# Kernel tuning notes

Hardware: AMD Instinct MI355X
Metric: run time of the kernel (lower is better)

## Reference

```python
import jax, jax.numpy as jnp
import numpy as np
import math

D_MODEL = 768
NHEAD = 12
NUM_LAYERS = 6
INPUT_DIM = 768
HEAD_DIM = D_MODEL // NHEAD
D_FF = 4 * D_MODEL
TOTAL_HEADS = NUM_LAYERS * NHEAD
B, N = 4, 512


def _ln(x, g, b, eps=1e-5):
    mu = jnp.mean(x, axis=-1, keepdims=True)
    var = jnp.mean((x - mu) ** 2, axis=-1, keepdims=True)
    return (x - mu) * jax.lax.rsqrt(var + eps) * g + b


def setup_inputs() -> dict:
    key = jax.random.key(0)
    ks = iter(jax.random.split(key, 32))
    s = 0.02  # init scale keeps sigmoid scores away from saturation
    d = {
        "sentence_embeddings": jax.random.normal(next(ks), (B, N, INPUT_DIM), jnp.float32),
        "Win": jax.random.normal(next(ks), (D_MODEL, INPUT_DIM), jnp.float32) * s,
        "b_in": jnp.zeros((D_MODEL,), jnp.float32),
        "Wq": jax.random.normal(next(ks), (NUM_LAYERS, D_MODEL, D_MODEL), jnp.float32) * s,
        "bq": jnp.zeros((NUM_LAYERS, D_MODEL), jnp.float32),
        "Wk": jax.random.normal(next(ks), (NUM_LAYERS, D_MODEL, D_MODEL), jnp.float32) * s,
        "bk": jnp.zeros((NUM_LAYERS, D_MODEL), jnp.float32),
        "Wv": jax.random.normal(next(ks), (NUM_LAYERS, D_MODEL, D_MODEL), jnp.float32) * s,
        "bv": jnp.zeros((NUM_LAYERS, D_MODEL), jnp.float32),
        "Wo": jax.random.normal(next(ks), (NUM_LAYERS, D_MODEL, D_MODEL), jnp.float32) * s,
        "bo": jnp.zeros((NUM_LAYERS, D_MODEL), jnp.float32),
        "g1": jnp.ones((NUM_LAYERS, D_MODEL), jnp.float32),
        "be1": jnp.zeros((NUM_LAYERS, D_MODEL), jnp.float32),
        "g2": jnp.ones((NUM_LAYERS, D_MODEL), jnp.float32),
        "be2": jnp.zeros((NUM_LAYERS, D_MODEL), jnp.float32),
        "W1": jax.random.normal(next(ks), (NUM_LAYERS, D_FF, D_MODEL), jnp.float32) * s,
        "bf1": jnp.zeros((NUM_LAYERS, D_FF), jnp.float32),
        "W2": jax.random.normal(next(ks), (NUM_LAYERS, D_MODEL, D_FF), jnp.float32) * s,
        "bf2": jnp.zeros((NUM_LAYERS, D_MODEL), jnp.float32),
        "Wr1": jax.random.normal(next(ks), (D_MODEL // 2, D_MODEL), jnp.float32) * s,
        "br1": jnp.zeros((D_MODEL // 2,), jnp.float32),
        "Wr2": jax.random.normal(next(ks), (TOTAL_HEADS, D_MODEL // 2), jnp.float32) * s,
        "br2": jnp.zeros((TOTAL_HEADS,), jnp.float32),
        "agg_bias": jnp.zeros((1,), jnp.float32),
    }
    return d


def _forward(sentence_embeddings, Win, b_in, Wq, bq, Wk, bk, Wv, bv, Wo, bo,
             g1, be1, g2, be2, W1, bf1, W2, bf2, Wr1, br1, Wr2, br2, agg_bias):
    b, n, _ = sentence_embeddings.shape
    x = sentence_embeddings @ Win.T + b_in  # [B,N,D]
    off_diag = (1.0 - jnp.eye(n, dtype=x.dtype))[None, None]  # [1,1,N,N]
    scale = 1.0 / math.sqrt(HEAD_DIM)
    all_scores = []
    for i in range(NUM_LAYERS):
        n1 = _ln(x, g1[i], be1[i])
        q = (n1 @ Wq[i].T + bq[i]).reshape(b, n, NHEAD, HEAD_DIM).transpose(0, 2, 1, 3)
        k = (n1 @ Wk[i].T + bk[i]).reshape(b, n, NHEAD, HEAD_DIM).transpose(0, 2, 1, 3)
        v = (n1 @ Wv[i].T + bv[i]).reshape(b, n, NHEAD, HEAD_DIM).transpose(0, 2, 1, 3)
        scores = jnp.einsum('bhnd,bhmd->bhnm', q, k) * scale
        probs = jax.nn.sigmoid(scores)  # [B,H,N,N]
        row_sums = probs.sum(axis=-1, keepdims=True) + 1e-6
        attn = jnp.einsum('bhnm,bhmd->bhnd', probs, v) / row_sums
        attn = attn.transpose(0, 2, 1, 3).reshape(b, n, D_MODEL)
        x = x + attn @ Wo[i].T + bo[i]
        n2 = _ln(x, g2[i], be2[i])
        ff = jax.nn.gelu(n2 @ W1[i].T + bf1[i], approximate=False) @ W2[i].T + bf2[i]
        x = x + ff
        all_scores.append(probs * off_diag)  # zero the diagonal
    raw_w = jax.nn.gelu(x @ Wr1.T + br1, approximate=False) @ Wr2.T + br2  # [B,N,LH]
    stacked = jnp.concatenate(all_scores, axis=1)  # [B, L*H, N, N]
    final = jnp.einsum('bnh,bhnm->bnm', raw_w, stacked)
    return final + agg_bias[0]


def reference(sentence_embeddings, Win, b_in, Wq, bq, Wk, bk, Wv, bv, Wo, bo,
              g1, be1, g2, be2, W1, bf1, W2, bf2, Wr1, br1, Wr2, br2, agg_bias):
    return _forward(sentence_embeddings, Win, b_in, Wq, bq, Wk, bk, Wv, bv, Wo, bo,
                    g1, be1, g2, be2, W1, bf1, W2, bf2, Wr1, br1, Wr2, br2, agg_bias)
```

## Files before the change

### kernel.cpp

```cpp
#include <hip/hip_runtime.h>
#include <stdint.h>

#define LAYERS 6
#define BB 4
#define NSEQ 512
#define DM 768
#define NH 12
#define HD 64
#define DFF 3072
#define MTOK 2048
#define QKVN 2304
#define DR1 384
#define TH 72

typedef __attribute__((ext_vector_type(8))) short bf16x8;
typedef __attribute__((ext_vector_type(4))) float f32x4;

__device__ __forceinline__ unsigned short f2bf(float f) {
  union { float f; uint32_t u; } v; v.f = f;
  return (unsigned short)((v.u + 0x7fffu + ((v.u >> 16) & 1u)) >> 16);
}
__device__ __forceinline__ float bf2f(unsigned short h) {
  union { uint32_t u; float f; } v; v.u = ((uint32_t)h) << 16;
  return v.f;
}
__device__ __forceinline__ void gload16(const void* g, void* l) {
  __builtin_amdgcn_global_load_lds((const __attribute__((address_space(1))) void*)g,
                                   (__attribute__((address_space(3))) void*)l, 16, 0, 0);
}
#define MFMA(a, b, c) __builtin_amdgcn_mfma_f32_16x16x32_bf16(a, b, c, 0, 0, 0)

__device__ __forceinline__ float sigmoid8(float s) {
  float e, r;
  float t = s * -0.18033688011112443f;
  asm("v_exp_f32 %0, %1" : "=v"(e) : "v"(t));
  float d = 1.0f + e;
  asm("v_rcp_f32 %0, %1" : "=v"(r) : "v"(d));
  return r;
}

__device__ __forceinline__ float gelu_f(float x) {
  float t = 0.7978845608028654f * x * (1.0f + 0.044715f * x * x);
  float u = fminf(t * 2.8853900817779268f, 126.0f);
  float e, r;
  asm("v_exp_f32 %0, %1" : "=v"(e) : "v"(u));
  float d = e + 1.0f;
  asm("v_rcp_f32 %0, %1" : "=v"(r) : "v"(d));
  return x * e * r;
}

__global__ void cvt_f32_bf16(const float* __restrict__ s, unsigned short* __restrict__ d, int n4) {
  int i = blockIdx.x * blockDim.x + threadIdx.x;
  if (i >= n4) return;
  float4 v = reinterpret_cast<const float4*>(s)[i];
  ushort4 o;
  o.x = f2bf(v.x); o.y = f2bf(v.y); o.z = f2bf(v.z); o.w = f2bf(v.w);
  reinterpret_cast<ushort4*>(d)[i] = o;
}

__global__ void convert_all(const float* __restrict__ Wq, const float* __restrict__ Wk,
                            const float* __restrict__ Wv, const float* __restrict__ Wo,
                            const float* __restrict__ W1, const float* __restrict__ W2,
                            const float* __restrict__ bqA, const float* __restrict__ bkA,
                            const float* __restrict__ bvA,
                            unsigned short* __restrict__ qkvw6, float* __restrict__ qkvb6,
                            unsigned short* __restrict__ wow6, unsigned short* __restrict__ w1w6,
                            unsigned short* __restrict__ w2w6) {
  const int A4 = (QKVN * DM) / 4;
  const int B4 = (DM * DM) / 4;
  const int C4 = (DFF * DM) / 4;
  const int l = blockIdx.y;
  const float* wq = Wq + (size_t)l * DM * DM;
  const float* wk = Wk + (size_t)l * DM * DM;
  const float* wv = Wv + (size_t)l * DM * DM;
  const float* wo = Wo + (size_t)l * DM * DM;
  const float* w1 = W1 + (size_t)l * DFF * DM;
  const float* w2 = W2 + (size_t)l * DM * DFF;
  unsigned short* qkvw = qkvw6 + (size_t)l * QKVN * DM;
  unsigned short* wow  = wow6  + (size_t)l * DM * DM;
  unsigned short* w1w  = w1w6  + (size_t)l * DFF * DM;
  unsigned short* w2w  = w2w6  + (size_t)l * DM * DFF;
  float* qkvb = qkvb6 + (size_t)l * QKVN;
  int i = blockIdx.x * blockDim.x + threadIdx.x;
  if (i < QKVN / 4) {
    int j = i * 4;
    #pragma unroll
    for (int t = 0; t < 4; ++t) {
      int jj = j + t;
      int seg = jj / DM, c = jj % DM;
      const float* src = (seg == 0) ? (bqA + l * DM) : ((seg == 1) ? (bkA + l * DM) : (bvA + l * DM));
      qkvb[jj] = src[c];
    }
  }
  const float* s4; unsigned short* dst;
  if (i < A4) {
    int j = i * 4; int row = j / DM; int c = j % DM;
    const float* w = (row < DM) ? wq : ((row < 2 * DM) ? wk : wv);
    s4 = w + (size_t)(row % DM) * DM + c; dst = qkvw + j;
  } else if (i < A4 + B4) {
    int j = (i - A4) * 4; s4 = wo + j; dst = wow + j;
  } else if (i < A4 + B4 + C4) {
    int j = (i - A4 - B4) * 4; s4 = w1 + j; dst = w1w + j;
  } else if (i < A4 + B4 + 2 * C4) {
    int j = (i - A4 - B4 - C4) * 4; s4 = w2 + j; dst = w2w + j;
  } else return;
  float4 v = *reinterpret_cast<const float4*>(s4);
  ushort4 o;
  o.x = f2bf(v.x); o.y = f2bf(v.y); o.z = f2bf(v.z); o.w = f2bf(v.w);
  *reinterpret_cast<ushort4*>(dst) = o;
}

__global__ __launch_bounds__(256) void ln_kernel(const float* __restrict__ x,
                                                 const float* __restrict__ g,
                                                 const float* __restrict__ b,
                                                 unsigned short* __restrict__ out) {
  int wave = threadIdx.x >> 6;
  int lane = threadIdx.x & 63;
  int row = blockIdx.x * 4 + wave;
  const float* xr = x + (size_t)row * DM;
  float v[12];
  #pragma unroll
  for (int c = 0; c < 3; ++c) {
    float4 t = *reinterpret_cast<const float4*>(xr + lane * 12 + c * 4);
    v[c * 4 + 0] = t.x; v[c * 4 + 1] = t.y; v[c * 4 + 2] = t.z; v[c * 4 + 3] = t.w;
  }
  float s = 0.f, s2 = 0.f;
  #pragma unroll
  for (int c = 0; c < 12; ++c) { s += v[c]; s2 += v[c] * v[c]; }
  #pragma unroll
  for (int m = 1; m < 64; m <<= 1) { s += __shfl_xor(s, m); s2 += __shfl_xor(s2, m); }
  float mu = s * (1.f / 768.f);
  float var = s2 * (1.f / 768.f) - mu * mu;
  float rstd = rsqrtf(var + 1e-5f);
  unsigned short o[12];
  #pragma unroll
  for (int c = 0; c < 12; ++c) {
    int col = lane * 12 + c;
    o[c] = f2bf((v[c] - mu) * rstd * g[col] + b[col]);
  }
  unsigned short* orow = out + (size_t)row * DM + lane * 12;
  #pragma unroll
  for (int c = 0; c < 3; ++c)
    reinterpret_cast<ushort4*>(orow)[c] = make_ushort4(o[c * 4], o[c * 4 + 1], o[c * 4 + 2], o[c * 4 + 3]);
}

__global__ __launch_bounds__(256) void ff2_ln(const float* __restrict__ pk,
                                              const float* __restrict__ bias,
                                              float* __restrict__ x,
                                              const float* __restrict__ g,
                                              const float* __restrict__ b,
                                              unsigned short* __restrict__ out,
                                              int last) {
  int wave = threadIdx.x >> 6;
  int lane = threadIdx.x & 63;
  int row = blockIdx.x * 4 + wave;
  size_t base = (size_t)row * DM;
  float v[12];
  #pragma unroll
  for (int c = 0; c < 3; ++c) {
    int col = lane * 12 + c * 4;
    float4 xv = *reinterpret_cast<const float4*>(x + base + col);
    float4 p0 = *reinterpret_cast<const float4*>(pk + base + col);
    float4 p1 = *reinterpret_cast<const float4*>(pk + (size_t)MTOK * DM + base + col);
    float4 bb = *reinterpret_cast<const float4*>(bias + col);
    v[c * 4 + 0] = xv.x + p0.x + p1.x + bb.x;
    v[c * 4 + 1] = xv.y + p0.y + p1.y + bb.y;
    v[c * 4 + 2] = xv.z + p0.z + p1.z + bb.z;
    v[c * 4 + 3] = xv.w + p0.w + p1.w + bb.w;
  }
  #pragma unroll
  for (int c = 0; c < 3; ++c) {
    float4 o = {v[c * 4], v[c * 4 + 1], v[c * 4 + 2], v[c * 4 + 3]};
    *reinterpret_cast<float4*>(x + base + lane * 12 + c * 4) = o;
  }
  unsigned short o[12];
  if (last) {
    #pragma unroll
    for (int c = 0; c < 12; ++c) o[c] = f2bf(v[c]);
  } else {
    float s = 0.f, s2 = 0.f;
    #pragma unroll
    for (int c = 0; c < 12; ++c) { s += v[c]; s2 += v[c] * v[c]; }
    #pragma unroll
    for (int m = 1; m < 64; m <<= 1) { s += __shfl_xor(s, m); s2 += __shfl_xor(s2, m); }
    float mu = s * (1.f / 768.f);
    float var = s2 * (1.f / 768.f) - mu * mu;
    float rstd = rsqrtf(var + 1e-5f);
    #pragma unroll
    for (int c = 0; c < 12; ++c) {
      int col = lane * 12 + c;
      o[c] = f2bf((v[c] - mu) * rstd * g[col] + b[col]);
    }
  }
  unsigned short* orow = out + base + lane * 12;
  #pragma unroll
  for (int c = 0; c < 3; ++c)
    reinterpret_cast<ushort4*>(orow)[c] = make_ushort4(o[c * 4], o[c * 4 + 1], o[c * 4 + 2], o[c * 4 + 3]);
}

template<int BM, int BN, int EPI>
__global__ __launch_bounds__(256) void gemm_bt(const unsigned short* __restrict__ A,
                                               const unsigned short* __restrict__ B,
                                               const float* __restrict__ bias,
                                               const float* __restrict__ resid,
                                               float* __restrict__ outf,
                                               unsigned short* __restrict__ outb,
                                               int M, int N, int K) {
  constexpr int MI = BM / 32;
  constexpr int NI = BN / 32;
  constexpr int ACH = BM / 32;
  constexpr int BCH = BN / 32;
  __shared__ unsigned short As[2][BM * 64];
  __shared__ unsigned short Bs[2][BN * 64];
  const int tid = threadIdx.x;
  const int w = tid >> 6, lane = tid & 63;
  const int wr = w >> 1, wc = w & 1;
  const int l15 = lane & 15, rq = lane >> 4;
  const int bM = blockIdx.y * BM, bN = blockIdx.x * BN;
  const f32x4 zero4 = {0.f, 0.f, 0.f, 0.f};
  f32x4 acc[MI][NI];
  #pragma unroll
  for (int mi = 0; mi < MI; ++mi)
    #pragma unroll
    for (int ni = 0; ni < NI; ++ni) acc[mi][ni] = zero4;
  const int srow = lane >> 3;
  const int scol = ((lane & 7) ^ (lane >> 3)) * 8;
  auto stage = [&](int bf, int k0) {
    #pragma unroll
    for (int cc = 0; cc < ACH; ++cc) {
      int c = w * ACH + cc;
      gload16(A + (size_t)(bM + 8 * c + srow) * K + k0 + scol, (void*)(&As[bf][c * 512]));
    }
    #pragma unroll
    for (int cc = 0; cc < BCH; ++cc) {
      int c = w * BCH + cc;
      gload16(B + (size_t)(bN + 8 * c + srow) * K + k0 + scol, (void*)(&Bs[bf][c * 512]));
    }
  };
  const int kper = K / gridDim.z;
  const int kbase = blockIdx.z * kper;
  const int nt = kper / 64;
  stage(0, kbase);
  __syncthreads();
  int buf = 0;
  for (int t = 0; t < nt; ++t) {
    if (t + 1 < nt) stage(buf ^ 1, kbase + (t + 1) * 64);
    #pragma unroll
    for (int kk = 0; kk < 2; ++kk) {
      bf16x8 af[MI], bfr[NI];
      #pragma unroll
      for (int mi = 0; mi < MI; ++mi) {
        int row = wr * (BM / 2) + mi * 16 + l15;
        af[mi] = *(const bf16x8*)(&As[buf][row * 64 + (((kk * 4 + rq) ^ (row & 7)) * 8)]);
      }
      #pragma unroll
      for (int ni = 0; ni < NI; ++ni) {
        int row = wc * (BN / 2) + ni * 16 + l15;
        bfr[ni] = *(const bf16x8*)(&Bs[buf][row * 64 + (((kk * 4 + rq) ^ (row & 7)) * 8)]);
      }
      #pragma unroll
      for (int mi = 0; mi < MI; ++mi)
        #pragma unroll
        for (int ni = 0; ni < NI; ++ni)
          acc[mi][ni] = MFMA(af[mi], bfr[ni], acc[mi][ni]);
    }
    __syncthreads();
    buf ^= 1;
  }
  #pragma unroll
  for (int mi = 0; mi < MI; ++mi)
    #pragma unroll
    for (int ni = 0; ni < NI; ++ni)
      #pragma unroll
      for (int r = 0; r < 4; ++r) {
        int row = bM + wr * (BM / 2) + mi * 16 + 4 * rq + r;
        int col = bN + wc * (BN / 2) + ni * 16 + l15;
        if constexpr (EPI == 4) {
          outf[(size_t)blockIdx.z * M * N + (size_t)row * N + col] = acc[mi][ni][r];
        } else {
          float val = acc[mi][ni][r] + bias[col];
          if constexpr (EPI == 0) {
            outb[(size_t)row * N + col] = f2bf(val);
          } else if constexpr (EPI == 1) {
            outb[(size_t)row * N + col] = f2bf(gelu_f(val));
          } else if constexpr (EPI == 2) {
            outf[(size_t)row * N + col] = resid[(size_t)row * N + col] + val;
          } else {
            outf[(size_t)row * N + col] = val;
          }
        }
      }
}

__global__ __launch_bounds__(256) void attn_kernel(const unsigned short* __restrict__ qkv,
                                                   float* __restrict__ po,
                                                   float* __restrict__ prs) {
  __shared__ unsigned short Ks[64 * 64];
  __shared__ unsigned short vt[64 * 72];
  __shared__ unsigned short pl[4][16 * 72];
  const int tid = threadIdx.x;
  const int w = tid >> 6, lane = tid & 63;
  const int l15 = lane & 15, rq = lane >> 4;
  const int b = blockIdx.y / NH, h = blockIdx.y % NH;
  const int n0 = blockIdx.x * 64;
  const int part = blockIdx.z;
  const unsigned short* base = qkv + (size_t)(b * NSEQ) * QKVN + h * HD;
  bf16x8 aq0, aq1;
  {
    const unsigned short* qp = base + (size_t)(n0 + w * 16 + l15) * QKVN + rq * 8;
    aq0 = *(const bf16x8*)qp;
    aq1 = *(const bf16x8*)(qp + 32);
  }
  float rs[4] = {0.f, 0.f, 0.f, 0.f};
  const f32x4 zero4 = {0.f, 0.f, 0.f, 0.f};
  f32x4 acco[4];
  #pragma unroll
  for (int j = 0; j < 4; ++j) acco[j] = zero4;
  unsigned short* plw = &pl[w][0];

  for (int mt = 0; mt < 4; ++mt) {
    const int m0 = part * 256 + mt * 64;
    __syncthreads();
    #pragma unroll
    for (int it = 0; it < 2; ++it) {
      int idx = tid + it * 256;
      int r = idx >> 3, c = idx & 7;
      bf16x8 kv = *(const bf16x8*)(base + 768 + (size_t)(m0 + r) * QKVN + c * 8);
      *(bf16x8*)(Ks + r * 64 + (c ^ (r & 7)) * 8) = kv;
      int cd = idx & 63, g = (idx >> 6) & 7;
      const unsigned short* vp = base + 1536 + (size_t)(m0 + g * 8) * QKVN + cd;
      bf16x8 vv;
      #pragma unroll
      for (int j = 0; j < 8; ++j) vv[j] = (short)vp[(size_t)j * QKVN];
      *(bf16x8*)(vt + cd * 72 + g * 8) = vv;
    }
    __syncthreads();
    #pragma unroll
    for (int ni = 0; ni < 4; ++ni) {
      int kr = ni * 16 + l15;
      bf16x8 bk0 = *(const bf16x8*)(Ks + kr * 64 + ((rq) ^ (kr & 7)) * 8);
      bf16x8 bk1 = *(const bf16x8*)(Ks + kr * 64 + ((rq + 4) ^ (kr & 7)) * 8);
      f32x4 z = zero4;
      z = MFMA(aq0, bk0, z);
      z = MFMA(aq1, bk1, z);
      #pragma unroll
      for (int r = 0; r < 4; ++r) {
        float p = sigmoid8(z[r]);
        rs[r] += p;
        plw[(4 * rq + r) * 72 + ni * 16 + l15] = f2bf(p);
      }
    }
    #pragma unroll
    for (int kk = 0; kk < 2; ++kk) {
      bf16x8 ap = *(const bf16x8*)(plw + l15 * 72 + kk * 32 + rq * 8);
      #pragma unroll
      for (int j2 = 0; j2 < 4; ++j2) {
        bf16x8 bvv = *(const bf16x8*)(vt + (j2 * 16 + l15) * 72 + kk * 32 + rq * 8);
        acco[j2] = MFMA(ap, bvv, acco[j2]);
      }
    }
  }
  #pragma unroll
  for (int m = 1; m < 16; m <<= 1)
    #pragma unroll
    for (int r = 0; r < 4; ++r) rs[r] += __shfl_xor(rs[r], m);
  float* pop = po + (size_t)part * MTOK * DM;
  #pragma unroll
  for (int j2 = 0; j2 < 4; ++j2)
    #pragma unroll
    for (int r = 0; r < 4; ++r) {
      int row = b * NSEQ + n0 + w * 16 + 4 * rq + r;
      int col = h * HD + j2 * 16 + l15;
      pop[(size_t)row * DM + col] = acco[j2][r];
    }
  if (l15 == 0) {
    #pragma unroll
    for (int r = 0; r < 4; ++r)
      prs[((size_t)part * (BB * NH) + blockIdx.y) * NSEQ + n0 + w * 16 + 4 * rq + r] = rs[r];
  }
}

__global__ __launch_bounds__(256) void attn_combine(const float* __restrict__ po,
                                                    const float* __restrict__ prs,
                                                    unsigned short* __restrict__ attnbf) {
  int i = blockIdx.x * 256 + threadIdx.x;
  int e = i * 4;
  int row = e / DM, col = e % DM;
  int b = row >> 9, n = row & 511, h = col >> 6;
  float r0 = prs[((size_t)(b * NH + h)) * NSEQ + n];
  float r1 = prs[(size_t)(BB * NH) * NSEQ + ((size_t)(b * NH + h)) * NSEQ + n];
  float inv = 1.f / (r0 + r1 + 1e-6f);
  float4 p0 = *reinterpret_cast<const float4*>(po + e);
  float4 p1 = *reinterpret_cast<const float4*>(po + (size_t)MTOK * DM + e);
  ushort4 o;
  o.x = f2bf((p0.x + p1.x) * inv);
  o.y = f2bf((p0.y + p1.y) * inv);
  o.z = f2bf((p0.z + p1.z) * inv);
  o.w = f2bf((p0.w + p1.w) * inv);
  *reinterpret_cast<ushort4*>(attnbf + e) = o;
}

__global__ __launch_bounds__(128) void wr2_kernel(const unsigned short* __restrict__ h1,
                                                  const float* __restrict__ wr2,
                                                  const float* __restrict__ br2,
                                                  float* __restrict__ raww) {
  __shared__ float hrow[DR1];
  int row = blockIdx.x;
  const unsigned short* hp = h1 + (size_t)row * DR1;
  for (int c = threadIdx.x; c < DR1; c += 128) hrow[c] = bf2f(hp[c]);
  __syncthreads();
  int j = threadIdx.x;
  if (j < TH) {
    const float* wrow = wr2 + (size_t)j * DR1;
    float acc = 0.f;
    for (int c4 = 0; c4 < DR1 / 4; ++c4) {
      float4 hv = *reinterpret_cast<const float4*>(hrow + c4 * 4);
      float4 wv = *reinterpret_cast<const float4*>(wrow + c4 * 4);
      acc += hv.x * wv.x + hv.y * wv.y + hv.z * wv.z + hv.w * wv.w;
    }
    raww[(size_t)row * TH + j] = acc + br2[j];
  }
}

__global__ __launch_bounds__(256) void agg_kernel(const unsigned short* __restrict__ qkv_all,
                                                  const float* __restrict__ raww,
                                                  float* __restrict__ part) {
  __shared__ unsigned short Ks[64 * 64];
  __shared__ unsigned short Qs[64 * 64];
  const int tid = threadIdx.x;
  const int w = tid >> 6, lane = tid & 63;
  const int l15 = lane & 15, rq = lane >> 4;
  const int z = blockIdx.z;
  const int l = z >> 2, b = z & 3;
  const int m0 = blockIdx.x * 64, nb = blockIdx.y * 64;
  const unsigned short* base = qkv_all + (size_t)l * MTOK * QKVN + (size_t)(b * NSEQ) * QKVN;
  const f32x4 zero4 = {0.f, 0.f, 0.f, 0.f};
  float acc[4][4];
  #pragma unroll
  for (int ni = 0; ni < 4; ++ni)
    #pragma unroll
    for (int r = 0; r < 4; ++r) acc[ni][r] = 0.f;
  for (int h = 0; h < NH; ++h) {
    __syncthreads();
    #pragma unroll
    for (int it = 0; it < 2; ++it) {
      int idx = tid + it * 256;
      int r = idx >> 3, c = idx & 7;
      bf16x8 kv = *(const bf16x8*)(base + (size_t)(m0 + r) * QKVN + 768 + h * HD + c * 8);
      *(bf16x8*)(Ks + r * 64 + (c ^ (r & 7)) * 8) = kv;
      bf16x8 qv = *(const bf16x8*)(base + (size_t)(nb + r) * QKVN + h * HD + c * 8);
      *(bf16x8*)(Qs + r * 64 + (c ^ (r & 7)) * 8) = qv;
    }
    __syncthreads();
    const int qr = w * 16 + l15;
    bf16x8 aq0 = *(const bf16x8*)(Qs + qr * 64 + ((rq) ^ (qr & 7)) * 8);
    bf16x8 aq1 = *(const bf16x8*)(Qs + qr * 64 + ((rq + 4) ^ (qr & 7)) * 8);
    float wl[4];
    #pragma unroll
    for (int r = 0; r < 4; ++r)
      wl[r] = raww[(size_t)(b * NSEQ + nb + w * 16 + 4 * rq + r) * TH + l * NH + h];
    #pragma unroll
    for (int ni = 0; ni < 4; ++ni) {
      int kr = ni * 16 + l15;
      bf16x8 bk0 = *(const bf16x8*)(Ks + kr * 64 + ((rq) ^ (kr & 7)) * 8);
      bf16x8 bk1 = *(const bf16x8*)(Ks + kr * 64 + ((rq + 4) ^ (kr & 7)) * 8);
      f32x4 zz = zero4;
      zz = MFMA(aq0, bk0, zz);
      zz = MFMA(aq1, bk1, zz);
      #pragma unroll
      for (int r = 0; r < 4; ++r) {
        acc[ni][r] += wl[r] * sigmoid8(zz[r]);
      }
    }
  }
  #pragma unroll
  for (int ni = 0; ni < 4; ++ni)
    #pragma unroll
    for (int r = 0; r < 4; ++r) {
      int n = nb + w * 16 + 4 * rq + r;
      part[((size_t)z * NSEQ + n) * NSEQ + m0 + ni * 16 + l15] = acc[ni][r];
    }
}

__global__ __launch_bounds__(256) void agg_reduce(const float* __restrict__ part,
                                                  const float* __restrict__ agg_bias,
                                                  float* __restrict__ out) {
  int i = blockIdx.x * 256 + threadIdx.x;
  int e = i * 4;
  float4 s = {0.f, 0.f, 0.f, 0.f};
  #pragma unroll
  for (int l = 0; l < LAYERS; ++l) {
    float4 p = *reinterpret_cast<const float4*>(part + (size_t)l * BB * NSEQ * NSEQ + e);
    s.x += p.x; s.y += p.y; s.z += p.z; s.w += p.w;
  }
  int n = (e >> 9) & 511, m = e & 511;
  float ab = agg_bias[0];
  float4 o;
  o.x = (n == m)     ? ab : s.x + ab;
  o.y = (n == m + 1) ? ab : s.y + ab;
  o.z = (n == m + 2) ? ab : s.z + ab;
  o.w = (n == m + 3) ? ab : s.w + ab;
  *reinterpret_cast<float4*>(out + e) = o;
}

extern "C" void kernel_launch(void* const* d_in, const int* in_sizes, int n_in,
                              void* d_out, int out_size, void* d_ws, size_t ws_size,
                              hipStream_t stream) {
  const float* emb  = (const float*)d_in[0];
  const float* Win  = (const float*)d_in[1];
  const float* b_in = (const float*)d_in[2];
  const float* Wq   = (const float*)d_in[3];
  const float* bq   = (const float*)d_in[4];
  const float* Wk   = (const float*)d_in[5];
  const float* bk   = (const float*)d_in[6];
  const float* Wv   = (const float*)d_in[7];
  const float* bv   = (const float*)d_in[8];
  const float* Wo   = (const float*)d_in[9];
  const float* bo   = (const float*)d_in[10];
  const float* g1   = (const float*)d_in[11];
  const float* be1  = (const float*)d_in[12];
  const float* g2   = (const float*)d_in[13];
  const float* be2  = (const float*)d_in[14];
  const float* W1   = (const float*)d_in[15];
  const float* bf1  = (const float*)d_in[16];
  const float* W2   = (const float*)d_in[17];
  const float* bf2  = (const float*)d_in[18];
  const float* Wr1  = (const float*)d_in[19];
  const float* br1  = (const float*)d_in[20];
  const float* Wr2  = (const float*)d_in[21];
  const float* br2  = (const float*)d_in[22];
  const float* aggb = (const float*)d_in[23];
  float* out = (float*)d_out;
  (void)in_sizes; (void)n_in; (void)out_size; (void)ws_size;

  char* ws = (char*)d_ws;
  size_t off = 0;
  auto alloc = [&](size_t bytes) -> char* {
    char* p = ws + off;
    off += (bytes + 255) & ~(size_t)255;
    return p;
  };
  unsigned short* qkvw6  = (unsigned short*)alloc((size_t)LAYERS * QKVN * DM * 2);
  float*          qkvb6  = (float*)alloc((size_t)LAYERS * QKVN * 4);
  unsigned short* wow6   = (unsigned short*)alloc((size_t)LAYERS * DM * DM * 2);
  unsigned short* w1w6   = (unsigned short*)alloc((size_t)LAYERS * DFF * DM * 2);
  unsigned short* w2w6   = (unsigned short*)alloc((size_t)LAYERS * DM * DFF * 2);
  unsigned short* winw   = (unsigned short*)alloc((size_t)DM * DM * 2);
  unsigned short* wr1w   = (unsigned short*)alloc((size_t)DR1 * DM * 2);
  unsigned short* h1bf   = (unsigned short*)alloc((size_t)MTOK * DR1 * 2);
  float*          raww   = (float*)alloc((size_t)MTOK * TH * 4);
  float*          prs    = (float*)alloc((size_t)2 * BB * NH * NSEQ * 4);
  float*          skbuf  = (float*)alloc((size_t)2 * MTOK * DM * 4);
  unsigned short* qkvall = (unsigned short*)alloc((size_t)LAYERS * MTOK * QKVN * 2);
  char* scratch = alloc(0);
  unsigned short* embbf  = (unsigned short*)(scratch);
  float*          x      = (float*)(scratch + 3145728);
  unsigned short* nbf    = (unsigned short*)(scratch + 3145728 + 6291456);
  unsigned short* attnbf = (unsigned short*)(scratch + 3145728 + 6291456 + 3145728);
  char*           S      = scratch + 3145728 + 6291456 + 3145728 + 3145728;
  unsigned short* xbf    = (unsigned short*)(S + 12582912);
  float*          po     = (float*)S;
  unsigned short* ff1bf  = (unsigned short*)S;
  float*          part   = (float*)scratch;

  cvt_f32_bf16<<<1536, 256, 0, stream>>>(emb, embbf, (MTOK * DM) / 4);
  cvt_f32_bf16<<<576, 256, 0, stream>>>(Win, winw, (DM * DM) / 4);
  cvt_f32_bf16<<<288, 256, 0, stream>>>(Wr1, wr1w, (DR1 * DM) / 4);

  const int CL_GRID = ((QKVN * DM + DM * DM + 2 * DFF * DM) / 4 + 255) / 256;
  convert_all<<<dim3(CL_GRID, LAYERS), 256, 0, stream>>>(Wq, Wk, Wv, Wo, W1, W2, bq, bk, bv,
                                                         qkvw6, qkvb6, wow6, w1w6, w2w6);

  dim3 g768(DM / 64, MTOK / 64);
  gemm_bt<64, 64, 3><<<g768, 256, 0, stream>>>(embbf, winw, b_in, nullptr, x, nullptr, MTOK, DM, DM);
  ln_kernel<<<512, 256, 0, stream>>>(x, g1, be1, nbf);

  for (int l = 0; l < LAYERS; ++l) {
    unsigned short* qkvl = qkvall + (size_t)l * MTOK * QKVN;
    dim3 gqkv(QKVN / 128, MTOK / 64);
    gemm_bt<64, 128, 0><<<gqkv, 256, 0, stream>>>(nbf, qkvw6 + (size_t)l * QKVN * DM,
                                                  qkvb6 + (size_t)l * QKVN, nullptr, nullptr,
                                                  qkvl, MTOK, QKVN, DM);
    attn_kernel<<<dim3(8, BB * NH, 2), 256, 0, stream>>>(qkvl, po, prs);
    attn_combine<<<(MTOK * DM / 4) / 256, 256, 0, stream>>>(po, prs, attnbf);
    gemm_bt<64, 64, 2><<<g768, 256, 0, stream>>>(attnbf, wow6 + (size_t)l * DM * DM,
                                                 bo + l * DM, x, x, nullptr, MTOK, DM, DM);
    ln_kernel<<<512, 256, 0, stream>>>(x, g2 + l * DM, be2 + l * DM, nbf);
    dim3 gff1(DFF / 128, MTOK / 64);
    gemm_bt<64, 128, 1><<<gff1, 256, 0, stream>>>(nbf, w1w6 + (size_t)l * DFF * DM,
                                                  bf1 + l * DFF, nullptr, nullptr, ff1bf,
                                                  MTOK, DFF, DM);
    dim3 gff2(DM / 64, MTOK / 64, 2);
    gemm_bt<64, 64, 4><<<gff2, 256, 0, stream>>>(ff1bf, w2w6 + (size_t)l * DM * DFF,
                                                 nullptr, nullptr, skbuf, nullptr, MTOK, DM, DFF);
    if (l < LAYERS - 1) {
      ff2_ln<<<512, 256, 0, stream>>>(skbuf, bf2 + l * DM, x,
                                      g1 + (l + 1) * DM, be1 + (l + 1) * DM, nbf, 0);
    } else {
      ff2_ln<<<512, 256, 0, stream>>>(skbuf, bf2 + l * DM, x, g1, be1, xbf, 1);
    }
  }

  dim3 gr1(DR1 / 64, MTOK / 64);
  gemm_bt<64, 64, 1><<<gr1, 256, 0, stream>>>(xbf, wr1w, br1, nullptr, nullptr, h1bf, MTOK, DR1, DM);
  wr2_kernel<<<MTOK, 128, 0, stream>>>(h1bf, Wr2, br2, raww);
  agg_kernel<<<dim3(8, 8, LAYERS * BB), 256, 0, stream>>>(qkvall, raww, part);
  agg_reduce<<<(BB * NSEQ * NSEQ / 4) / 256, 256, 0, stream>>>(part, aggb, out);
}
```

Baseline: 707.4 us.

## Fuse weight fp32-to-bf16 conversion into GEMM B loads and merge attention split-K in-block

Removes the separate weight conversion kernels. The GEMMs now read fp32 weights directly, converting them to bf16 in registers with packed cvt before writing to LDS, and the QKV GEMM selects the Q/K/V weight and bias segment per tile. Attention now splits the key range across waves inside one block and combines the partial results through shared memory, which eliminates the attn_combine kernel and its fp32 partial buffers. In exchange, each GEMM reads twice the weight bytes and does extra conversion work on every tile. The B operand also moves from the asynchronous global-to-LDS path to register staging.

New measurement: 849.4 us. 20.1% more time.

```diff
diff --git a/kernel.cpp b/kernel.cpp
--- a/kernel.cpp
+++ b/kernel.cpp
@@ -15,6 +15,7 @@
 
 typedef __attribute__((ext_vector_type(8))) short bf16x8;
 typedef __attribute__((ext_vector_type(4))) float f32x4;
+typedef __attribute__((ext_vector_type(4))) unsigned int u32x4;
 
 __device__ __forceinline__ unsigned short f2bf(float f) {
   union { float f; uint32_t u; } v; v.f = f;
@@ -23,6 +24,11 @@
 __device__ __forceinline__ float bf2f(unsigned short h) {
   union { uint32_t u; float f; } v; v.u = ((uint32_t)h) << 16;
   return v.f;
+}
+__device__ __forceinline__ uint32_t pkbf(float lo, float hi) {
+  uint32_t r;
+  asm("v_cvt_pk_bf16_f32 %0, %1, %2" : "=v"(r) : "v"(lo), "v"(hi));
+  return r;
 }
 __device__ __forceinline__ void gload16(const void* g, void* l) {
   __builtin_amdgcn_global_load_lds((const __attribute__((address_space(1))) void*)g,
@@ -56,58 +62,6 @@
   ushort4 o;
   o.x = f2bf(v.x); o.y = f2bf(v.y); o.z = f2bf(v.z); o.w = f2bf(v.w);
   reinterpret_cast<ushort4*>(d)[i] = o;
-}
-
-__global__ void convert_all(const float* __restrict__ Wq, const float* __restrict__ Wk,
-                            const float* __restrict__ Wv, const float* __restrict__ Wo,
-                            const float* __restrict__ W1, const float* __restrict__ W2,
-                            const float* __restrict__ bqA, const float* __restrict__ bkA,
-                            const float* __restrict__ bvA,
-                            unsigned short* __restrict__ qkvw6, float* __restrict__ qkvb6,
-                            unsigned short* __restrict__ wow6, unsigned short* __restrict__ w1w6,
-                            unsigned short* __restrict__ w2w6) {
-  const int A4 = (QKVN * DM) / 4;
-  const int B4 = (DM * DM) / 4;
-  const int C4 = (DFF * DM) / 4;
-  const int l = blockIdx.y;
-  const float* wq = Wq + (size_t)l * DM * DM;
-  const float* wk = Wk + (size_t)l * DM * DM;
-  const float* wv = Wv + (size_t)l * DM * DM;
-  const float* wo = Wo + (size_t)l * DM * DM;
-  const float* w1 = W1 + (size_t)l * DFF * DM;
-  const float* w2 = W2 + (size_t)l * DM * DFF;
-  unsigned short* qkvw = qkvw6 + (size_t)l * QKVN * DM;
-  unsigned short* wow  = wow6  + (size_t)l * DM * DM;
-  unsigned short* w1w  = w1w6  + (size_t)l * DFF * DM;
-  unsigned short* w2w  = w2w6  + (size_t)l * DM * DFF;
-  float* qkvb = qkvb6 + (size_t)l * QKVN;
-  int i = blockIdx.x * blockDim.x + threadIdx.x;
-  if (i < QKVN / 4) {
-    int j = i * 4;
-    #pragma unroll
-    for (int t = 0; t < 4; ++t) {
-      int jj = j + t;
-      int seg = jj / DM, c = jj % DM;
-      const float* src = (seg == 0) ? (bqA + l * DM) : ((seg == 1) ? (bkA + l * DM) : (bvA + l * DM));
-      qkvb[jj] = src[c];
-    }
-  }
-  const float* s4; unsigned short* dst;
-  if (i < A4) {
-    int j = i * 4; int row = j / DM; int c = j % DM;
-    const float* w = (row < DM) ? wq : ((row < 2 * DM) ? wk : wv);
-    s4 = w + (size_t)(row % DM) * DM + c; dst = qkvw + j;
-  } else if (i < A4 + B4) {
-    int j = (i - A4) * 4; s4 = wo + j; dst = wow + j;
-  } else if (i < A4 + B4 + C4) {
-    int j = (i - A4 - B4) * 4; s4 = w1 + j; dst = w1w + j;
-  } else if (i < A4 + B4 + 2 * C4) {
-    int j = (i - A4 - B4 - C4) * 4; s4 = w2 + j; dst = w2w + j;
-  } else return;
-  float4 v = *reinterpret_cast<const float4*>(s4);
-  ushort4 o;
-  o.x = f2bf(v.x); o.y = f2bf(v.y); o.z = f2bf(v.z); o.w = f2bf(v.w);
-  *reinterpret_cast<ushort4*>(dst) = o;
 }
 
 __global__ __launch_bounds__(256) void ln_kernel(const float* __restrict__ x,
@@ -198,10 +152,14 @@
     reinterpret_cast<ushort4*>(orow)[c] = make_ushort4(o[c * 4], o[c * 4 + 1], o[c * 4 + 2], o[c * 4 + 3]);
 }
 
-template<int BM, int BN, int EPI>
+template<int BM, int BN, int EPI, bool SEG3>
 __global__ __launch_bounds__(256) void gemm_bt(const unsigned short* __restrict__ A,
-                                               const unsigned short* __restrict__ B,
-                                               const float* __restrict__ bias,
+                                               const float* __restrict__ B0,
+                                               const float* __restrict__ B1,
+                                               const float* __restrict__ B2,
+                                               const float* __restrict__ bias0,
+                                               const float* __restrict__ bias1,
+                                               const float* __restrict__ bias2,
                                                const float* __restrict__ resid,
                                                float* __restrict__ outf,
                                                unsigned short* __restrict__ outb,
@@ -216,7 +174,16 @@
   const int w = tid >> 6, lane = tid & 63;
   const int wr = w >> 1, wc = w & 1;
   const int l15 = lane & 15, rq = lane >> 4;
-  const int bM = blockIdx.y * BM, bN = blockIdx.x * BN;
+  const int bM = blockIdx.y * BM, bNg = blockIdx.x * BN;
+  const float* Bp; const float* biasp; int bNl;
+  if constexpr (SEG3) {
+    int seg = bNg / 768;
+    Bp    = (seg == 0) ? B0 : ((seg == 1) ? B1 : B2);
+    biasp = (seg == 0) ? bias0 : ((seg == 1) ? bias1 : bias2);
+    bNl = bNg - seg * 768;
+  } else {
+    Bp = B0; biasp = bias0; bNl = bNg;
+  }
   const f32x4 zero4 = {0.f, 0.f, 0.f, 0.f};
   f32x4 acc[MI][NI];
   #pragma unroll
@@ -224,27 +191,48 @@
     #pragma unroll
     for (int ni = 0; ni < NI; ++ni) acc[mi][ni] = zero4;
   const int srow = lane >> 3;
-  const int scol = ((lane & 7) ^ (lane >> 3)) * 8;
-  auto stage = [&](int bf, int k0) {
+  const int jj = lane & 7;
+  const int scolA = (jj ^ srow) * 8;
+  float4 bq0[BCH], bq1[BCH];
+  auto stageA = [&](int bf, int k0) {
     #pragma unroll
     for (int cc = 0; cc < ACH; ++cc) {
       int c = w * ACH + cc;
-      gload16(A + (size_t)(bM + 8 * c + srow) * K + k0 + scol, (void*)(&As[bf][c * 512]));
-    }
+      gload16(A + (size_t)(bM + 8 * c + srow) * K + k0 + scolA, (void*)(&As[bf][c * 512]));
+    }
+  };
+  auto loadB = [&](int k0) {
     #pragma unroll
     for (int cc = 0; cc < BCH; ++cc) {
       int c = w * BCH + cc;
-      gload16(B + (size_t)(bN + 8 * c + srow) * K + k0 + scol, (void*)(&Bs[bf][c * 512]));
+      const float* src = Bp + (size_t)(bNl + 8 * c + srow) * K + k0 + jj * 8;
+      bq0[cc] = *reinterpret_cast<const float4*>(src);
+      bq1[cc] = *reinterpret_cast<const float4*>(src + 4);
+    }
+  };
+  auto writeB = [&](int bf) {
+    #pragma unroll
+    for (int cc = 0; cc < BCH; ++cc) {
+      int c = w * BCH + cc;
+      u32x4 pv;
+      pv.x = pkbf(bq0[cc].x, bq0[cc].y);
+      pv.y = pkbf(bq0[cc].z, bq0[cc].w);
+      pv.z = pkbf(bq1[cc].x, bq1[cc].y);
+      pv.w = pkbf(bq1[cc].z, bq1[cc].w);
+      *reinterpret_cast<u32x4*>(&Bs[bf][c * 512 + srow * 64 + ((jj ^ srow) * 8)]) = pv;
     }
   };
   const int kper = K / gridDim.z;
   const int kbase = blockIdx.z * kper;
   const int nt = kper / 64;
-  stage(0, kbase);
+  stageA(0, kbase);
+  loadB(kbase);
+  writeB(0);
   __syncthreads();
   int buf = 0;
   for (int t = 0; t < nt; ++t) {
-    if (t + 1 < nt) stage(buf ^ 1, kbase + (t + 1) * 64);
+    bool pre = (t + 1 < nt);
+    if (pre) { loadB(kbase + (t + 1) * 64); stageA(buf ^ 1, kbase + (t + 1) * 64); }
     #pragma unroll
     for (int kk = 0; kk < 2; ++kk) {
       bf16x8 af[MI], bfr[NI];
@@ -264,6 +252,7 @@
         for (int ni = 0; ni < NI; ++ni)
           acc[mi][ni] = MFMA(af[mi], bfr[ni], acc[mi][ni]);
     }
+    if (pre) writeB(buf ^ 1);
     __syncthreads();
     buf ^= 1;
   }
@@ -274,40 +263,42 @@
       #pragma unroll
       for (int r = 0; r < 4; ++r) {
         int row = bM + wr * (BM / 2) + mi * 16 + 4 * rq + r;
-        int col = bN + wc * (BN / 2) + ni * 16 + l15;
+        int colL = bNl + wc * (BN / 2) + ni * 16 + l15;
+        int colG = bNg + wc * (BN / 2) + ni * 16 + l15;
         if constexpr (EPI == 4) {
-          outf[(size_t)blockIdx.z * M * N + (size_t)row * N + col] = acc[mi][ni][r];
+          outf[(size_t)blockIdx.z * M * N + (size_t)row * N + colG] = acc[mi][ni][r];
         } else {
-          float val = acc[mi][ni][r] + bias[col];
+          float val = acc[mi][ni][r] + biasp[colL];
           if constexpr (EPI == 0) {
-            outb[(size_t)row * N + col] = f2bf(val);
+            outb[(size_t)row * N + colG] = f2bf(val);
           } else if constexpr (EPI == 1) {
-            outb[(size_t)row * N + col] = f2bf(gelu_f(val));
+            outb[(size_t)row * N + colG] = f2bf(gelu_f(val));
           } else if constexpr (EPI == 2) {
-            outf[(size_t)row * N + col] = resid[(size_t)row * N + col] + val;
+            outf[(size_t)row * N + colG] = resid[(size_t)row * N + colG] + val;
           } else {
-            outf[(size_t)row * N + col] = val;
+            outf[(size_t)row * N + colG] = val;
           }
         }
       }
 }
 
 __global__ __launch_bounds__(256) void attn_kernel(const unsigned short* __restrict__ qkv,
-                                                   float* __restrict__ po,
-                                                   float* __restrict__ prs) {
-  __shared__ unsigned short Ks[64 * 64];
-  __shared__ unsigned short vt[64 * 72];
+                                                   unsigned short* __restrict__ attnbf) {
+  __shared__ unsigned short Ks[2][64 * 64];
+  __shared__ unsigned short vt[2][64 * 72];
   __shared__ unsigned short pl[4][16 * 72];
+  __shared__ float cmb[2][64 * 16];
   const int tid = threadIdx.x;
   const int w = tid >> 6, lane = tid & 63;
   const int l15 = lane & 15, rq = lane >> 4;
+  const int qsub = w & 1, ksub = w >> 1;
+  const int hid = tid & 127;
   const int b = blockIdx.y / NH, h = blockIdx.y % NH;
-  const int n0 = blockIdx.x * 64;
-  const int part = blockIdx.z;
+  const int n0 = blockIdx.x * 32 + qsub * 16;
   const unsigned short* base = qkv + (size_t)(b * NSEQ) * QKVN + h * HD;
   bf16x8 aq0, aq1;
   {
-    const unsigned short* qp = base + (size_t)(n0 + w * 16 + l15) * QKVN + rq * 8;
+    const unsigned short* qp = base + (size_t)(n0 + l15) * QKVN + rq * 8;
     aq0 = *(const bf16x8*)qp;
     aq1 = *(const bf16x8*)(qp + 32);
   }
@@ -317,29 +308,31 @@
   #pragma unroll
   for (int j = 0; j < 4; ++j) acco[j] = zero4;
   unsigned short* plw = &pl[w][0];
+  unsigned short* Ksh = &Ks[ksub][0];
+  unsigned short* vth = &vt[ksub][0];
 
   for (int mt = 0; mt < 4; ++mt) {
-    const int m0 = part * 256 + mt * 64;
+    const int m0 = ksub * 256 + mt * 64;
     __syncthreads();
     #pragma unroll
-    for (int it = 0; it < 2; ++it) {
-      int idx = tid + it * 256;
+    for (int it = 0; it < 4; ++it) {
+      int idx = hid + it * 128;
       int r = idx >> 3, c = idx & 7;
       bf16x8 kv = *(const bf16x8*)(base + 768 + (size_t)(m0 + r) * QKVN + c * 8);
-      *(bf16x8*)(Ks + r * 64 + (c ^ (r & 7)) * 8) = kv;
+      *(bf16x8*)(Ksh + r * 64 + ((c ^ (r & 7)) * 8)) = kv;
       int cd = idx & 63, g = (idx >> 6) & 7;
       const unsigned short* vp = base + 1536 + (size_t)(m0 + g * 8) * QKVN + cd;
       bf16x8 vv;
       #pragma unroll
       for (int j = 0; j < 8; ++j) vv[j] = (short)vp[(size_t)j * QKVN];
-      *(bf16x8*)(vt + cd * 72 + g * 8) = vv;
+      *(bf16x8*)(vth + cd * 72 + g * 8) = vv;
     }
     __syncthreads();
     #pragma unroll
     for (int ni = 0; ni < 4; ++ni) {
       int kr = ni * 16 + l15;
-      bf16x8 bk0 = *(const bf16x8*)(Ks + kr * 64 + ((rq) ^ (kr & 7)) * 8);
-      bf16x8 bk1 = *(const bf16x8*)(Ks + kr * 64 + ((rq + 4) ^ (kr & 7)) * 8);
+      bf16x8 bk0 = *(const bf16x8*)(Ksh + kr * 64 + ((rq ^ (kr & 7)) * 8));
+      bf16x8 bk1 = *(const bf16x8*)(Ksh + kr * 64 + (((rq + 4) ^ (kr & 7)) * 8));
       f32x4 z = zero4;
       z = MFMA(aq0, bk0, z);
       z = MFMA(aq1, bk1, z);
@@ -355,49 +348,40 @@
       bf16x8 ap = *(const bf16x8*)(plw + l15 * 72 + kk * 32 + rq * 8);
       #pragma unroll
       for (int j2 = 0; j2 < 4; ++j2) {
-        bf16x8 bvv = *(const bf16x8*)(vt + (j2 * 16 + l15) * 72 + kk * 32 + rq * 8);
+        bf16x8 bvv = *(const bf16x8*)(vth + (j2 * 16 + l15) * 72 + kk * 32 + rq * 8);
         acco[j2] = MFMA(ap, bvv, acco[j2]);
       }
     }
   }
-  #pragma unroll
-  for (int m = 1; m < 16; m <<= 1)
-    #pragma unroll
-    for (int r = 0; r < 4; ++r) rs[r] += __shfl_xor(rs[r], m);
-  float* pop = po + (size_t)part * MTOK * DM;
-  #pragma unroll
-  for (int j2 = 0; j2 < 4; ++j2)
-    #pragma unroll
-    for (int r = 0; r < 4; ++r) {
-      int row = b * NSEQ + n0 + w * 16 + 4 * rq + r;
-      int col = h * HD + j2 * 16 + l15;
-      pop[(size_t)row * DM + col] = acco[j2][r];
-    }
-  if (l15 == 0) {
-    #pragma unroll
-    for (int r = 0; r < 4; ++r)
-      prs[((size_t)part * (BB * NH) + blockIdx.y) * NSEQ + n0 + w * 16 + 4 * rq + r] = rs[r];
-  }
-}
-
-__global__ __launch_bounds__(256) void attn_combine(const float* __restrict__ po,
-                                                    const float* __restrict__ prs,
-                                                    unsigned short* __restrict__ attnbf) {
-  int i = blockIdx.x * 256 + threadIdx.x;
-  int e = i * 4;
-  int row = e / DM, col = e % DM;
-  int b = row >> 9, n = row & 511, h = col >> 6;
-  float r0 = prs[((size_t)(b * NH + h)) * NSEQ + n];
-  float r1 = prs[(size_t)(BB * NH) * NSEQ + ((size_t)(b * NH + h)) * NSEQ + n];
-  float inv = 1.f / (r0 + r1 + 1e-6f);
-  float4 p0 = *reinterpret_cast<const float4*>(po + e);
-  float4 p1 = *reinterpret_cast<const float4*>(po + (size_t)MTOK * DM + e);
-  ushort4 o;
-  o.x = f2bf((p0.x + p1.x) * inv);
-  o.y = f2bf((p0.y + p1.y) * inv);
-  o.z = f2bf((p0.z + p1.z) * inv);
-  o.w = f2bf((p0.w + p1.w) * inv);
-  *reinterpret_cast<ushort4*>(attnbf + e) = o;
+  __syncthreads();
+  float* rsx = (float*)&pl[0][0];
+  if (ksub == 1) {
+    float* c0 = &cmb[qsub][lane * 16];
+    #pragma unroll
+    for (int j2 = 0; j2 < 4; ++j2)
+      #pragma unroll
+      for (int r = 0; r < 4; ++r) c0[j2 * 4 + r] = acco[j2][r];
+    #pragma unroll
+    for (int r = 0; r < 4; ++r) rsx[qsub * 256 + lane * 4 + r] = rs[r];
+  }
+  __syncthreads();
+  if (ksub == 0) {
+    const float* c0 = &cmb[qsub][lane * 16];
+    #pragma unroll
+    for (int r = 0; r < 4; ++r) rs[r] += rsx[qsub * 256 + lane * 4 + r];
+    #pragma unroll
+    for (int m = 1; m < 16; m <<= 1)
+      #pragma unroll
+      for (int r = 0; r < 4; ++r) rs[r] += __shfl_xor(rs[r], m);
+    #pragma unroll
+    for (int j2 = 0; j2 < 4; ++j2)
+      #pragma unroll
+      for (int r = 0; r < 4; ++r) {
+        int row = b * NSEQ + n0 + 4 * rq + r;
+        int col = h * HD + j2 * 16 + l15;
+        attnbf[(size_t)row * DM + col] = f2bf((acco[j2][r] + c0[j2 * 4 + r]) / (rs[r] + 1e-6f));
+      }
+  }
 }
 
 __global__ __launch_bounds__(128) void wr2_kernel(const unsigned short* __restrict__ h1,
@@ -540,16 +524,8 @@
     off += (bytes + 255) & ~(size_t)255;
     return p;
   };
-  unsigned short* qkvw6  = (unsigned short*)alloc((size_t)LAYERS * QKVN * DM * 2);
-  float*          qkvb6  = (float*)alloc((size_t)LAYERS * QKVN * 4);
-  unsigned short* wow6   = (unsigned short*)alloc((size_t)LAYERS * DM * DM * 2);
-  unsigned short* w1w6   = (unsigned short*)alloc((size_t)LAYERS * DFF * DM * 2);
-  unsigned short* w2w6   = (unsigned short*)alloc((size_t)LAYERS * DM * DFF * 2);
-  unsigned short* winw   = (unsigned short*)alloc((size_t)DM * DM * 2);
-  unsigned short* wr1w   = (unsigned short*)alloc((size_t)DR1 * DM * 2);
   unsigned short* h1bf   = (unsigned short*)alloc((size_t)MTOK * DR1 * 2);
   float*          raww   = (float*)alloc((size_t)MTOK * TH * 4);
-  float*          prs    = (float*)alloc((size_t)2 * BB * NH * NSEQ * 4);
   float*          skbuf  = (float*)alloc((size_t)2 * MTOK * DM * 4);
   unsigned short* qkvall = (unsigned short*)alloc((size_t)LAYERS * MTOK * QKVN * 2);
   char* scratch = alloc(0);
@@ -557,42 +533,42 @@
   float*          x      = (float*)(scratch + 3145728);
   unsigned short* nbf    = (unsigned short*)(scratch + 3145728 + 6291456);
   unsigned short* attnbf = (unsigned short*)(scratch + 3145728 + 6291456 + 3145728);
-  char*           S      = scratch + 3145728 + 6291456 + 3145728 + 3145728;
-  unsigned short* xbf    = (unsigned short*)(S + 12582912);
-  float*          po     = (float*)S;
-  unsigned short* ff1bf  = (unsigned short*)S;
+  unsigned short* ff1bf  = (unsigned short*)(scratch + 3145728 + 6291456 + 3145728 + 3145728);
+  unsigned short* xbf    = (unsigned short*)(scratch + 3145728 + 6291456 + 3145728 + 3145728 + 12582912);
   float*          part   = (float*)scratch;
 
   cvt_f32_bf16<<<1536, 256, 0, stream>>>(emb, embbf, (MTOK * DM) / 4);
-  cvt_f32_bf16<<<576, 256, 0, stream>>>(Win, winw, (DM * DM) / 4);
-  cvt_f32_bf16<<<288, 256, 0, stream>>>(Wr1, wr1w, (DR1 * DM) / 4);
-
-  const int CL_GRID = ((QKVN * DM + DM * DM + 2 * DFF * DM) / 4 + 255) / 256;
-  convert_all<<<dim3(CL_GRID, LAYERS), 256, 0, stream>>>(Wq, Wk, Wv, Wo, W1, W2, bq, bk, bv,
-                                                         qkvw6, qkvb6, wow6, w1w6, w2w6);
 
   dim3 g768(DM / 64, MTOK / 64);
-  gemm_bt<64, 64, 3><<<g768, 256, 0, stream>>>(embbf, winw, b_in, nullptr, x, nullptr, MTOK, DM, DM);
+  gemm_bt<64, 64, 3, false><<<g768, 256, 0, stream>>>(embbf, Win, Win, Win, b_in, b_in, b_in,
+                                                      nullptr, x, nullptr, MTOK, DM, DM);
   ln_kernel<<<512, 256, 0, stream>>>(x, g1, be1, nbf);
 
   for (int l = 0; l < LAYERS; ++l) {
     unsigned short* qkvl = qkvall + (size_t)l * MTOK * QKVN;
+    const float* wq = Wq + (size_t)l * DM * DM;
+    const float* wk = Wk + (size_t)l * DM * DM;
+    const float* wv = Wv + (size_t)l * DM * DM;
     dim3 gqkv(QKVN / 128, MTOK / 64);
-    gemm_bt<64, 128, 0><<<gqkv, 256, 0, stream>>>(nbf, qkvw6 + (size_t)l * QKVN * DM,
-                                                  qkvb6 + (size_t)l * QKVN, nullptr, nullptr,
-                                                  qkvl, MTOK, QKVN, DM);
-    attn_kernel<<<dim3(8, BB * NH, 2), 256, 0, stream>>>(qkvl, po, prs);
-    attn_combine<<<(MTOK * DM / 4) / 256, 256, 0, stream>>>(po, prs, attnbf);
-    gemm_bt<64, 64, 2><<<g768, 256, 0, stream>>>(attnbf, wow6 + (size_t)l * DM * DM,
-                                                 bo + l * DM, x, x, nullptr, MTOK, DM, DM);
+    gemm_bt<64, 128, 0, true><<<gqkv, 256, 0, stream>>>(nbf, wq, wk, wv,
+                                                        bq + l * DM, bk + l * DM, bv + l * DM,
+                                                        nullptr, nullptr, qkvl, MTOK, QKVN, DM);
+    attn_kernel<<<dim3(NSEQ / 32, BB * NH), 256, 0, stream>>>(qkvl, attnbf);
+    const float* wo = Wo + (size_t)l * DM * DM;
+    gemm_bt<64, 64, 2, false><<<g768, 256, 0, stream>>>(attnbf, wo, wo, wo,
+                                                        bo + l * DM, nullptr, nullptr,
+                                                        x, x, nullptr, MTOK, DM, DM);
     ln_kernel<<<512, 256, 0, stream>>>(x, g2 + l * DM, be2 + l * DM, nbf);
+    const float* w1 = W1 + (size_t)l * DFF * DM;
     dim3 gff1(DFF / 128, MTOK / 64);
-    gemm_bt<64, 128, 1><<<gff1, 256, 0, stream>>>(nbf, w1w6 + (size_t)l * DFF * DM,
-                                                  bf1 + l * DFF, nullptr, nullptr, ff1bf,
-                                                  MTOK, DFF, DM);
+    gemm_bt<64, 128, 1, false><<<gff1, 256, 0, stream>>>(nbf, w1, w1, w1,
+                                                         bf1 + l * DFF, nullptr, nullptr,
+                                                         nullptr, nullptr, ff1bf, MTOK, DFF, DM);
+    const float* w2 = W2 + (size_t)l * DM * DFF;
     dim3 gff2(DM / 64, MTOK / 64, 2);
-    gemm_bt<64, 64, 4><<<gff2, 256, 0, stream>>>(ff1bf, w2w6 + (size_t)l * DM * DFF,
-                                                 nullptr, nullptr, skbuf, nullptr, MTOK, DM, DFF);
+    gemm_bt<64, 64, 4, false><<<gff2, 256, 0, stream>>>(ff1bf, w2, w2, w2,
+                                                        nullptr, nullptr, nullptr,
+                                                        nullptr, skbuf, nullptr, MTOK, DM, DFF);
     if (l < LAYERS - 1) {
       ff2_ln<<<512, 256, 0, stream>>>(skbuf, bf2 + l * DM, x,
                                       g1 + (l + 1) * DM, be1 + (l + 1) * DM, nbf, 0);
@@ -602,7 +578,8 @@
   }
 
   dim3 gr1(DR1 / 64, MTOK / 64);
-  gemm_bt<64, 64, 1><<<gr1, 256, 0, stream>>>(xbf, wr1w, br1, nullptr, nullptr, h1bf, MTOK, DR1, DM);
+  gemm_bt<64, 64, 1, false><<<gr1, 256, 0, stream>>>(xbf, Wr1, Wr1, Wr1, br1, br1, br1,
+                                                     nullptr, nullptr, h1bf, MTOK, DR1, DM);
   wr2_kernel<<<MTOK, 128, 0, stream>>>(h1bf, Wr2, br2, raww);
   agg_kernel<<<dim3(8, 8, LAYERS * BB), 256, 0, stream>>>(qkvall, raww, part);
   agg_reduce<<<(BB * NSEQ * NSEQ / 4) / 256, 256, 0, stream>>>(part, aggb, out);
```
